# Optimization experiments

Hardware: AMD Instinct MI355X
Metric: run time of the kernel (lower is better)

## Reference

```python
import jax, jax.numpy as jnp
import numpy as np

NEG_INF = -1e30  # stand-in for float('-inf') that is safe under softmax


def setup_inputs() -> dict:
    key = jax.random.key(0)
    k1, k2, k3, k4 = jax.random.split(key, 4)
    B, T, C, H = 4, 4096, 1024, 128
    x = jax.random.normal(k1, (B, T, C), dtype=jnp.float32)
    # nn.Linear(n_emb, head_size, bias=False): store as [C, H] so y = x @ W
    Wk = jax.random.normal(k2, (C, H), dtype=jnp.float32) * (C ** -0.5)
    Wq = jax.random.normal(k3, (C, H), dtype=jnp.float32) * (C ** -0.5)
    Wv = jax.random.normal(k4, (C, H), dtype=jnp.float32) * (C ** -0.5)
    return {"x": x, "Wk": Wk, "Wq": Wq, "Wv": Wv}


def reference(x, Wk, Wq, Wv):
    B, T, C = x.shape
    k = x @ Wk  # [B, T, H]
    q = x @ Wq  # [B, T, H]
    v = x @ Wv  # [B, T, H]
    # Faithful to original: wei = k @ q^T, scaled by C**-0.5 (C = n_emb)
    wei = jnp.einsum('bih,bjh->bij', k, q) * (C ** -0.5)  # [B, T, T]
    causal = jnp.tril(jnp.ones((T, T), dtype=bool))
    wei = jnp.where(causal, wei, NEG_INF)
    wei = jax.nn.softmax(wei, axis=-1)
    out = jnp.einsum('bij,bjh->bih', wei, v)  # [B, T, H]
    return out
```

## Files before the change

### kernel.cpp

```cpp
#include <hip/hip_runtime.h>
#include <hip/hip_bf16.h>

#define T_SEQ 4096
#define NBATCH 4
#define C_EMB 1024
#define H_DIM 128
#define M_ROWS (NBATCH * T_SEQ)
#define SPLIT 4

typedef __bf16 bf16x8 __attribute__((ext_vector_type(8)));
typedef float  floatx4 __attribute__((ext_vector_type(4)));

__device__ __forceinline__ ushort f2bf(float f) {
    __hip_bfloat16 h = __float2bfloat16(f);
    return *reinterpret_cast<ushort*>(&h);
}
__device__ __forceinline__ float bf2f(ushort u) {
    unsigned int v = ((unsigned int)u) << 16;
    return *reinterpret_cast<float*>(&v);
}
__device__ __forceinline__ uint4 pack8(const float4& a, const float4& b) {
    __hip_bfloat162 h0 = __float22bfloat162_rn(make_float2(a.x, a.y));
    __hip_bfloat162 h1 = __float22bfloat162_rn(make_float2(a.z, a.w));
    __hip_bfloat162 h2 = __float22bfloat162_rn(make_float2(b.x, b.y));
    __hip_bfloat162 h3 = __float22bfloat162_rn(make_float2(b.z, b.w));
    uint4 r;
    r.x = *reinterpret_cast<unsigned int*>(&h0);
    r.y = *reinterpret_cast<unsigned int*>(&h1);
    r.z = *reinterpret_cast<unsigned int*>(&h2);
    r.w = *reinterpret_cast<unsigned int*>(&h3);
    return r;
}
__device__ __forceinline__ void gld16(const ushort* g, ushort* l) {
    __builtin_amdgcn_global_load_lds(
        (const __attribute__((address_space(1))) unsigned int*)(g),
        (__attribute__((address_space(3))) unsigned int*)(l),
        16, 0, 0);
}

__global__ __launch_bounds__(256) void transpose_w(
    const float* __restrict__ Wk, const float* __restrict__ Wq,
    const float* __restrict__ Wv, ushort* __restrict__ wt) {
    const int z = blockIdx.y;
    const float* W = (z == 0) ? Wk : (z == 1) ? Wq : Wv;
    ushort* Wtz = wt + (size_t)z * H_DIM * C_EMB;
    int linear = blockIdx.x * 256 + threadIdx.x;
    int n  = linear >> 7;
    int k0 = (linear & 127) << 3;
    ushort tmp[8];
#pragma unroll
    for (int j = 0; j < 8; ++j)
        tmp[j] = f2bf(W[(size_t)(k0 + j) * H_DIM + n]);
    uint4 pk;
    pk.x = (unsigned int)tmp[0] | ((unsigned int)tmp[1] << 16);
    pk.y = (unsigned int)tmp[2] | ((unsigned int)tmp[3] << 16);
    pk.z = (unsigned int)tmp[4] | ((unsigned int)tmp[5] << 16);
    pk.w = (unsigned int)tmp[6] | ((unsigned int)tmp[7] << 16);
    *reinterpret_cast<uint4*>(Wtz + (size_t)n * C_EMB + k0) = pk;
}

__global__ __launch_bounds__(512, 2) void qkv_gemm(
    const float* __restrict__ x, const ushort* __restrict__ wt,
    ushort* __restrict__ kqv) {
    const int m0 = blockIdx.x * 64;

    __shared__ ushort As[64 * 64];
    __shared__ ushort Bs[384 * 64];

    const int tid  = threadIdx.x;
    const int lane = tid & 63;
    const int wave = tid >> 6;
    const int l15  = lane & 15;
    const int quad = lane >> 4;
    const int mg   = (wave >> 1) * 16;
    const int nb   = (wave & 1) * 12;

    floatx4 acc[12];
#pragma unroll
    for (int nj = 0; nj < 12; ++nj) acc[nj] = floatx4{0.f, 0.f, 0.f, 0.f};

    const int ar = tid >> 3;
    const int ac = tid & 7;
    const float* xrow = x + (size_t)(m0 + ar) * C_EMB + ac * 8;
    float4 xa = *reinterpret_cast<const float4*>(xrow);
    float4 xb = *reinterpret_cast<const float4*>(xrow + 4);

    for (int kt = 0; kt < 16; ++kt) {
        __syncthreads();
#pragma unroll
        for (int i = 0; i < 6; ++i) {
            int rbase = wave * 48 + i * 8;
            int row = rbase + (lane >> 3);
            int chg = (lane & 7) ^ (row & 7);
            gld16(wt + (size_t)row * C_EMB + kt * 64 + chg * 8,
                  Bs + rbase * 64);
        }
        {
            int chp = ac ^ (ar & 7);
            *reinterpret_cast<uint4*>(As + ar * 64 + chp * 8) = pack8(xa, xb);
        }
        __syncthreads();

        if (kt < 15) {
            const float* nsrc = xrow + (kt + 1) * 64;
            xa = *reinterpret_cast<const float4*>(nsrc);
            xb = *reinterpret_cast<const float4*>(nsrc + 4);
        }

#pragma unroll
        for (int kk = 0; kk < 2; ++kk) {
            bf16x8 a = *reinterpret_cast<const bf16x8*>(
                As + (mg + l15) * 64 + ((4 * kk + quad) ^ (l15 & 7)) * 8);
#pragma unroll
            for (int nj = 0; nj < 12; ++nj) {
                int brow = (nb + nj) * 16 + l15;
                bf16x8 b = *reinterpret_cast<const bf16x8*>(
                    Bs + brow * 64 + ((4 * kk + quad) ^ (brow & 7)) * 8);
                acc[nj] = __builtin_amdgcn_mfma_f32_16x16x32_bf16(a, b, acc[nj], 0, 0, 0);
            }
        }
    }

    const int rowb = m0 + mg + quad * 4;
#pragma unroll
    for (int nj = 0; nj < 12; ++nj) {
        int gcol = (nb + nj) * 16 + l15;
        int z = gcol >> 7;
        int cz = gcol & 127;
        if (z < 2) {
            const float scale = (z == 0) ? 0.03125f : 1.0f;
            ushort* outz = kqv + (size_t)z * M_ROWS * H_DIM;
#pragma unroll
            for (int r = 0; r < 4; ++r)
                outz[(size_t)(rowb + r) * H_DIM + cz] = f2bf(acc[nj][r] * scale);
        } else {
            ushort* vt = kqv + (size_t)2 * M_ROWS * H_DIM;
            int bb   = rowb >> 12;
            int tloc = rowb & (T_SEQ - 1);
            ushort4 pk;
            pk.x = f2bf(acc[nj][0]);
            pk.y = f2bf(acc[nj][1]);
            pk.z = f2bf(acc[nj][2]);
            pk.w = f2bf(acc[nj][3]);
            *reinterpret_cast<ushort4*>(
                vt + ((size_t)(bb * H_DIM + cz) << 12) + tloc) = pk;
        }
    }
}

#define P_STRIDE 72
__global__ __launch_bounds__(256, 3) void flash_chunk(
    const ushort* __restrict__ kqv, ushort* __restrict__ partO,
    float* __restrict__ partML) {
    const int it = blockIdx.x >> 2;
    const int c  = blockIdx.x & 3;
    if (c > it) return;
    const int b  = blockIdx.y;
    const int i0 = it * 64;

    const ushort* Qg = kqv + (size_t)b * T_SEQ * H_DIM;
    const ushort* Kg = kqv + (size_t)M_ROWS * H_DIM + (size_t)b * T_SEQ * H_DIM;
    const ushort* Vt = kqv + (size_t)2 * M_ROWS * H_DIM + (size_t)b * H_DIM * T_SEQ;

    __shared__ ushort Ks[64 * 128];
    __shared__ ushort Vs[128 * 64];
    __shared__ ushort Ps[4][16 * P_STRIDE];

    const int tid  = threadIdx.x;
    const int lane = tid & 63;
    const int wave = tid >> 6;
    const int l15  = lane & 15;
    const int quad = lane >> 4;

    bf16x8 q[4];
    {
        const ushort* qrow = Qg + (size_t)(i0 + wave * 16 + l15) * H_DIM + quad * 8;
#pragma unroll
        for (int kk = 0; kk < 4; ++kk)
            q[kk] = *reinterpret_cast<const bf16x8*>(qrow + kk * 32);
    }

    float m_i[4], l_i[4];
#pragma unroll
    for (int r = 0; r < 4; ++r) { m_i[r] = -1e30f; l_i[r] = 0.f; }
    floatx4 o[8];
#pragma unroll
    for (int nh = 0; nh < 8; ++nh) o[nh] = floatx4{0.f, 0.f, 0.f, 0.f};

    ushort* Pw = Ps[wave];

    for (int jt = c; jt <= it; jt += SPLIT) {
        const int j0 = jt * 64;
        __syncthreads();
#pragma unroll
        for (int i = 0; i < 4; ++i) {
            int row = wave * 16 + i * 4 + (lane >> 4);
            int chg = (lane & 15) ^ (row & 15);
            gld16(Kg + (size_t)(j0 + row) * H_DIM + chg * 8,
                  Ks + (wave * 16 + i * 4) * 128);
        }
#pragma unroll
        for (int i = 0; i < 4; ++i) {
            int row = wave * 32 + i * 8 + (lane >> 3);
            int chg = (lane & 7) ^ (row & 7);
            gld16(Vt + (size_t)row * T_SEQ + j0 + chg * 8,
                  Vs + (wave * 32 + i * 8) * 64);
        }
        __syncthreads();

        floatx4 s[4];
#pragma unroll
        for (int ni = 0; ni < 4; ++ni) s[ni] = floatx4{0.f, 0.f, 0.f, 0.f};
#pragma unroll
        for (int kk = 0; kk < 4; ++kk)
#pragma unroll
            for (int ni = 0; ni < 4; ++ni) {
                bf16x8 kb = *reinterpret_cast<const bf16x8*>(
                    Ks + (ni * 16 + l15) * 128 + ((4 * kk + quad) ^ l15) * 8);
                s[ni] = __builtin_amdgcn_mfma_f32_16x16x32_bf16(q[kk], kb, s[ni], 0, 0, 0);
            }

        if (jt == it) {
            int ii = i0 + wave * 16 + quad * 4;
#pragma unroll
            for (int ni = 0; ni < 4; ++ni) {
                int j = j0 + ni * 16 + l15;
#pragma unroll
                for (int r = 0; r < 4; ++r)
                    if (j > ii + r) s[ni][r] = -1e30f;
            }
        }

        float alpha[4], rs[4];
#pragma unroll
        for (int r = 0; r < 4; ++r) {
            float v = fmaxf(fmaxf(s[0][r], s[1][r]), fmaxf(s[2][r], s[3][r]));
#pragma unroll
            for (int off = 8; off >= 1; off >>= 1)
                v = fmaxf(v, __shfl_xor(v, off, 64));
            float mn = fmaxf(m_i[r], v);
            alpha[r] = __expf(m_i[r] - mn);
            m_i[r] = mn;
            rs[r] = 0.f;
        }
#pragma unroll
        for (int ni = 0; ni < 4; ++ni)
#pragma unroll
            for (int r = 0; r < 4; ++r) {
                float p = __expf(s[ni][r] - m_i[r]);
                rs[r] += p;
                Pw[(quad * 4 + r) * P_STRIDE + ni * 16 + l15] = f2bf(p);
            }
#pragma unroll
        for (int r = 0; r < 4; ++r) {
            float v = rs[r];
#pragma unroll
            for (int off = 8; off >= 1; off >>= 1)
                v += __shfl_xor(v, off, 64);
            l_i[r] = l_i[r] * alpha[r] + v;
        }
#pragma unroll
        for (int nh = 0; nh < 8; ++nh)
#pragma unroll
            for (int r = 0; r < 4; ++r) o[nh][r] *= alpha[r];

#pragma unroll
        for (int kp = 0; kp < 2; ++kp) {
            bf16x8 a = *reinterpret_cast<const bf16x8*>(
                Pw + l15 * P_STRIDE + kp * 32 + quad * 8);
#pragma unroll
            for (int nh = 0; nh < 8; ++nh) {
                bf16x8 vb = *reinterpret_cast<const bf16x8*>(
                    Vs + (nh * 16 + l15) * 64 + ((4 * kp + quad) ^ (l15 & 7)) * 8);
                o[nh] = __builtin_amdgcn_mfma_f32_16x16x32_bf16(a, vb, o[nh], 0, 0, 0);
            }
        }
    }

    const int idx = ((b * 64 + it) << 2) + c;
    ushort* po = partO + (size_t)idx * 64 * 128;
#pragma unroll
    for (int nh = 0; nh < 8; ++nh)
#pragma unroll
        for (int r = 0; r < 4; ++r) {
            int row = wave * 16 + quad * 4 + r;
            po[(size_t)row * 128 + nh * 16 + l15] = f2bf(o[nh][r]);
        }
    if (l15 == 0) {
        float* ml = partML + (size_t)idx * 128;
#pragma unroll
        for (int r = 0; r < 4; ++r) {
            int row = wave * 16 + quad * 4 + r;
            ml[row]      = m_i[r];
            ml[64 + row] = l_i[r];
        }
    }
}

__global__ __launch_bounds__(256) void combine(
    const ushort* __restrict__ partO, const float* __restrict__ partML,
    float* __restrict__ out) {
    const int it = blockIdx.x, b = blockIdx.y;
    const int count = min(SPLIT, it + 1);
    const int tid = threadIdx.x;
    const int row = tid >> 2;
    const int cg  = (tid & 3) * 32;
    const int base = (b * 64 + it) << 2;

    float m_c[SPLIT], l_c[SPLIT];
    float M = -1e30f;
    for (int cc = 0; cc < count; ++cc) {
        const float* ml = partML + (size_t)(base + cc) * 128;
        m_c[cc] = ml[row];
        l_c[cc] = ml[64 + row];
        M = fmaxf(M, m_c[cc]);
    }
    float L = 0.f, w[SPLIT];
    for (int cc = 0; cc < count; ++cc) {
        w[cc] = __expf(m_c[cc] - M);
        L += w[cc] * l_c[cc];
    }

    float acc[32];
#pragma unroll
    for (int j = 0; j < 32; ++j) acc[j] = 0.f;
    for (int cc = 0; cc < count; ++cc) {
        const ushort* po = partO + (size_t)(base + cc) * 8192 + (size_t)row * 128 + cg;
        float wc = w[cc];
#pragma unroll
        for (int g = 0; g < 4; ++g) {
            uint4 v = *reinterpret_cast<const uint4*>(po + g * 8);
            const ushort* pv = reinterpret_cast<const ushort*>(&v);
#pragma unroll
            for (int e = 0; e < 8; ++e)
                acc[g * 8 + e] += wc * bf2f(pv[e]);
        }
    }
    float invL = 1.0f / L;
    float* op = out + ((size_t)b * T_SEQ + it * 64 + row) * H_DIM + cg;
#pragma unroll
    for (int g = 0; g < 8; ++g) {
        float4 v;
        v.x = acc[g * 4 + 0] * invL;
        v.y = acc[g * 4 + 1] * invL;
        v.z = acc[g * 4 + 2] * invL;
        v.w = acc[g * 4 + 3] * invL;
        *reinterpret_cast<float4*>(op + g * 4) = v;
    }
}

extern "C" void kernel_launch(void* const* d_in, const int* in_sizes, int n_in,
                              void* d_out, int out_size, void* d_ws, size_t ws_size,
                              hipStream_t stream) {
    const float* x  = (const float*)d_in[0];
    const float* Wk = (const float*)d_in[1];
    const float* Wq = (const float*)d_in[2];
    const float* Wv = (const float*)d_in[3];

    ushort* kqv    = (ushort*)d_ws;
    ushort* wt     = kqv + (size_t)3 * M_ROWS * H_DIM;
    ushort* partO  = wt + (size_t)3 * H_DIM * C_EMB;
    float*  partML = (float*)(partO + (size_t)1024 * 64 * 128);

    transpose_w<<<dim3(64, 3), 256, 0, stream>>>(Wk, Wq, Wv, wt);
    qkv_gemm<<<dim3(256), 512, 0, stream>>>(x, wt, kqv);
    flash_chunk<<<dim3(64 * SPLIT, NBATCH), 256, 0, stream>>>(kqv, partO, partML);
    combine<<<dim3(64, NBATCH), 256, 0, stream>>>(partO, partML, (float*)d_out);
}
```

Measured before the change: 182.6 us.

## Prefetch next K/V tile into registers and skip rescale when max unchanged

Replaces the direct global-to-LDS loads with register staging. The next K/V tile is loaded into registers while the current tile is computed, then written to swizzled LDS at the top of the next iteration, so global latency overlaps with the MFMA work. It also skips the online-softmax rescale of O and l when no row's running max grows, guarded by a wave-wide __any check. The cost is more VGPRs for the staging buffers, which may lower occupancy, plus a divergent branch.

Result: slower. 254.0 us (+39.1%).

```diff
diff --git a/kernel.cpp b/kernel.cpp
--- a/kernel.cpp
+++ b/kernel.cpp
@@ -189,24 +189,48 @@
 
     ushort* Pw = Ps[wave];
 
+    uint4 kreg[4], vreg[4];
+    auto loadKV = [&](int jt) {
+        const int j0s = jt * 64;
+#pragma unroll
+        for (int i = 0; i < 4; ++i) {
+            int u = i * 256 + tid;
+            int kr = u >> 4, kch = u & 15;
+            kreg[i] = *reinterpret_cast<const uint4*>(
+                Kg + (size_t)(j0s + kr) * H_DIM + kch * 8);
+        }
+#pragma unroll
+        for (int i = 0; i < 4; ++i) {
+            int u = i * 256 + tid;
+            int vr = u >> 3, vch = u & 7;
+            vreg[i] = *reinterpret_cast<const uint4*>(
+                Vt + (size_t)vr * T_SEQ + j0s + vch * 8);
+        }
+    };
+    auto writeKV = [&]() {
+#pragma unroll
+        for (int i = 0; i < 4; ++i) {
+            int u = i * 256 + tid;
+            int kr = u >> 4, kch = u & 15;
+            *reinterpret_cast<uint4*>(Ks + kr * 128 + (kch ^ (kr & 15)) * 8) = kreg[i];
+        }
+#pragma unroll
+        for (int i = 0; i < 4; ++i) {
+            int u = i * 256 + tid;
+            int vr = u >> 3, vch = u & 7;
+            *reinterpret_cast<uint4*>(Vs + vr * 64 + (vch ^ (vr & 7)) * 8) = vreg[i];
+        }
+    };
+
+    loadKV(c);
+
     for (int jt = c; jt <= it; jt += SPLIT) {
         const int j0 = jt * 64;
         __syncthreads();
-#pragma unroll
-        for (int i = 0; i < 4; ++i) {
-            int row = wave * 16 + i * 4 + (lane >> 4);
-            int chg = (lane & 15) ^ (row & 15);
-            gld16(Kg + (size_t)(j0 + row) * H_DIM + chg * 8,
-                  Ks + (wave * 16 + i * 4) * 128);
-        }
-#pragma unroll
-        for (int i = 0; i < 4; ++i) {
-            int row = wave * 32 + i * 8 + (lane >> 3);
-            int chg = (lane & 7) ^ (row & 7);
-            gld16(Vt + (size_t)row * T_SEQ + j0 + chg * 8,
-                  Vs + (wave * 32 + i * 8) * 64);
-        }
+        writeKV();
         __syncthreads();
+
+        if (jt + SPLIT <= it) loadKV(jt + SPLIT);
 
         floatx4 s[4];
 #pragma unroll
@@ -231,18 +255,30 @@
             }
         }
 
-        float alpha[4], rs[4];
+        float vmax[4], rs[4];
+        bool grow = false;
 #pragma unroll
         for (int r = 0; r < 4; ++r) {
             float v = fmaxf(fmaxf(s[0][r], s[1][r]), fmaxf(s[2][r], s[3][r]));
 #pragma unroll
             for (int off = 8; off >= 1; off >>= 1)
                 v = fmaxf(v, __shfl_xor(v, off, 64));
-            float mn = fmaxf(m_i[r], v);
-            alpha[r] = __expf(m_i[r] - mn);
-            m_i[r] = mn;
-            rs[r] = 0.f;
-        }
+            vmax[r] = v;
+            grow = grow || (v > m_i[r]);
+        }
+        if (__any(grow)) {
+#pragma unroll
+            for (int r = 0; r < 4; ++r) {
+                float mn = fmaxf(m_i[r], vmax[r]);
+                float alpha = __expf(m_i[r] - mn);
+                m_i[r] = mn;
+                l_i[r] *= alpha;
+#pragma unroll
+                for (int nh = 0; nh < 8; ++nh) o[nh][r] *= alpha;
+            }
+        }
+#pragma unroll
+        for (int r = 0; r < 4; ++r) rs[r] = 0.f;
 #pragma unroll
         for (int ni = 0; ni < 4; ++ni)
 #pragma unroll
@@ -257,12 +293,8 @@
 #pragma unroll
             for (int off = 8; off >= 1; off >>= 1)
                 v += __shfl_xor(v, off, 64);
-            l_i[r] = l_i[r] * alpha[r] + v;
-        }
-#pragma unroll
-        for (int nh = 0; nh < 8; ++nh)
-#pragma unroll
-            for (int r = 0; r < 4; ++r) o[nh][r] *= alpha[r];
+            l_i[r] += v;
+        }
 
 #pragma unroll
         for (int kp = 0; kp < 2; ++kp) {
```
